# Kernel tuning notes

Measured on AMD Instinct MI355X. Metric: run time of the kernel, lower is better.

Reference implementation:

```python
import jax, jax.numpy as jnp
import numpy as np

N = 100000
E = 1600000
NEG_SLOPE = 0.2


def _gat_layer(x, src, dst, W, a_src, a_dst, b, heads, out_ch):
    n = x.shape[0]
    h = (x @ W).reshape(n, heads, out_ch)                      # [N,H,C]
    alpha_src = (h * a_src).sum(-1)                            # [N,H]
    alpha_dst = (h * a_dst).sum(-1)                            # [N,H]
    e = jax.nn.leaky_relu(alpha_src[src] + alpha_dst[dst], NEG_SLOPE)  # [E,H]
    # segment softmax over incoming edges of each destination node
    m = jax.ops.segment_max(e, dst, num_segments=n)            # [N,H]
    ex = jnp.exp(e - m[dst])
    denom = jax.ops.segment_sum(ex, dst, num_segments=n)       # [N,H]
    alpha = ex / (denom[dst] + 1e-16)                          # [E,H]
    msg = h[src] * alpha[:, :, None]                           # [E,H,C]
    out = jax.ops.segment_sum(msg, dst, num_segments=n)        # [N,H,C]
    return out.reshape(n, heads * out_ch) + b


def setup_inputs() -> dict:
    key = jax.random.key(0)
    ks = jax.random.split(key, 10)
    glorot = lambda k, shape: jax.random.normal(k, shape, jnp.float32) * np.sqrt(2.0 / (shape[0] + shape[-1]))
    x = jax.random.normal(ks[0], (N, 5), jnp.float32)
    edge_index = jax.random.randint(ks[1], (2, E), 0, N, jnp.int64)
    return {
        "x": x,
        "edge_index": edge_index,
        "W1": glorot(ks[2], (5, 64)),
        "a_src1": glorot(ks[3], (8, 8)),
        "a_dst1": glorot(ks[4], (8, 8)),
        "b1": jnp.zeros((64,), jnp.float32),
        "W2": glorot(ks[5], (64, 2)),
        "a_src2": glorot(ks[6], (1, 2)),
        "a_dst2": glorot(ks[7], (1, 2)),
        "b2": jnp.zeros((2,), jnp.float32),
    }


def reference(x, edge_index, W1, a_src1, a_dst1, b1, W2, a_src2, a_dst2, b2):
    n = x.shape[0]
    loop = jnp.arange(n, dtype=edge_index.dtype)
    src = jnp.concatenate([edge_index[0], loop])   # PyG GATConv adds self-loops
    dst = jnp.concatenate([edge_index[1], loop])
    # dropout layers are no-ops in eval mode
    h = jax.nn.elu(_gat_layer(x, src, dst, W1, a_src1, a_dst1, b1, heads=8, out_ch=8))
    out = _gat_layer(h, src, dst, W2, a_src2, a_dst2, b2, heads=1, out_ch=2)
    return jax.nn.log_softmax(out, axis=1)
```

## Files before the change

kernel.cpp:

```cpp
#include <hip/hip_runtime.h>
#include <hip/hip_fp16.h>
#include <math.h>
#include <stdint.h>

#define N_NODES 100000
#define N_EDGES 1600000
#define N_TOT   (N_EDGES + N_NODES)
#define NEG_SLOPE 0.2f
#define LOG2E 1.44269504088896340736f

#define CB     128
#define CBBITS 7
#define NCB    ((N_NODES + CB - 1) / CB)
#define TP     2048
#define NPB    ((N_EDGES + TP - 1) / TP)
#define WINB   2560

typedef int nt_int4 __attribute__((ext_vector_type(4)));

__global__ void k_node1(const float* __restrict__ x, const float* __restrict__ W1,
                        const float* __restrict__ a_src1, const float* __restrict__ a_dst1,
                        __half* __restrict__ xh, __half* __restrict__ as1h,
                        float* __restrict__ ad1) {
    int tid  = blockIdx.x * blockDim.x + threadIdx.x;
    int n    = tid >> 3;
    int head = tid & 7;
    if (n >= N_NODES) return;

    float xv[5];
#pragma unroll
    for (int k = 0; k < 5; ++k) xv[k] = x[n * 5 + k];

    float as = 0.f, ad = 0.f;
#pragma unroll
    for (int j = 0; j < 8; ++j) {
        int c = head * 8 + j;
        float acc = 0.f;
#pragma unroll
        for (int k = 0; k < 5; ++k) acc += xv[k] * W1[k * 64 + c];
        as += acc * a_src1[c];
        ad += acc * a_dst1[c];
    }
    as1h[n * 8 + head] = __float2half(as * LOG2E);
    ad1[n * 8 + head] = ad * LOG2E;

    if (head == 0) {
        __half2 p0 = __halves2half2(__float2half(xv[0]), __float2half(xv[1]));
        __half2 p1 = __halves2half2(__float2half(xv[2]), __float2half(xv[3]));
        __half2 p2 = __halves2half2(__float2half(xv[4]), __float2half(0.f));
        __half2 p3 = __halves2half2(__float2half(0.f), __float2half(0.f));
        __half2* xp = (__half2*)&xh[(size_t)n * 8];
        xp[0] = p0; xp[1] = p1; xp[2] = p2; xp[3] = p3;
    }
}

__global__ void __launch_bounds__(512) k_part(
        const int* __restrict__ src, const int* __restrict__ dst,
        int* __restrict__ ofsT, unsigned* __restrict__ pairs) {
    __shared__ int lcnt[1024];
    __shared__ int sm[512];
    __shared__ unsigned stage[TP];
    int blk = blockIdx.x;
    int t = threadIdx.x;
    int base = blk * TP + t * 4;
    bool act = base < N_EDGES;
    int nE = min(TP, N_EDGES - blk * TP);

    lcnt[t] = 0; lcnt[t + 512] = 0;
    __syncthreads();

    nt_int4 s4, d4;
    if (act) {
        s4 = __builtin_nontemporal_load((const nt_int4*)(src + base));
        d4 = __builtin_nontemporal_load((const nt_int4*)(dst + base));
#pragma unroll
        for (int j = 0; j < 4; ++j) atomicAdd(&lcnt[d4[j] >> CBBITS], 1);
    }
    __syncthreads();

    int b0 = lcnt[t * 2], b1 = lcnt[t * 2 + 1];
    int local = b0 + b1;
    sm[t] = local;
    __syncthreads();
    for (int off = 1; off < 512; off <<= 1) {
        int u = (t >= off) ? sm[t - off] : 0;
        __syncthreads();
        sm[t] += u;
        __syncthreads();
    }
    int run = sm[t] - local;
    lcnt[t * 2] = run; lcnt[t * 2 + 1] = run + b0;
    if (t * 2     <= NCB) ofsT[(size_t)(t * 2)     * NPB + blk] = run;
    if (t * 2 + 1 <= NCB) ofsT[(size_t)(t * 2 + 1) * NPB + blk] = run + b0;
    __syncthreads();

    if (act) {
#pragma unroll
        for (int j = 0; j < 4; ++j) {
            int d = d4[j], s = s4[j];
            int bin = d >> CBBITS;
            int idx = atomicAdd(&lcnt[bin], 1);
            stage[idx] = ((unsigned)(d & (CB - 1)) << 17) | (unsigned)s;
        }
    }
    __syncthreads();
    for (int i = t; i < nE; i += 512)
        pairs[(size_t)blk * TP + i] = stage[i];
}

__global__ void __launch_bounds__(512) k_csr(
        const int* __restrict__ ofsT, const unsigned* __restrict__ pairs,
        int* __restrict__ rbeg, int* __restrict__ rend, int* __restrict__ ssrc) {
    __shared__ unsigned stIn[WINB];
    __shared__ int stOut[WINB];
    __shared__ int lcnt[CB], lofs[CB], lcur[CB];
    __shared__ int wsum[2];
    __shared__ int acur;
    int B = blockIdx.x, t = threadIdx.x;
    int nvalid = min(CB, N_NODES - B * CB);
    int obase = B * WINB;

    if (t < CB) {
        lcnt[t] = (t < nvalid) ? 1 : 0;
        lcur[t] = 1;
    }
    if (t == 0) acur = 0;
    __syncthreads();

    for (int blk = t; blk < NPB; blk += 512) {
        int o0 = ofsT[(size_t)B       * NPB + blk];
        int o1 = ofsT[(size_t)(B + 1) * NPB + blk];
        int n = o1 - o0;
        if (n > 0) {
            int p = atomicAdd(&acur, n);
            const unsigned* pp = pairs + (size_t)blk * TP + o0;
            for (int i = 0; i < n; ++i) {
                unsigned r = pp[i];
                stIn[p + i] = r;
                atomicAdd(&lcnt[r >> 17], 1);
            }
        }
    }
    __syncthreads();
    int m = acur;

    int v = (t < CB) ? lcnt[t] : 0;
    int ln = t & 63, wv = t >> 6;
    int sc = v;
#pragma unroll
    for (int off = 1; off < 64; off <<= 1) {
        int u = __shfl_up(sc, off, 64);
        if (ln >= off) sc += u;
    }
    if (ln == 63 && wv < 2) wsum[wv] = sc;
    __syncthreads();
    int wbase = (wv == 1) ? wsum[0] : 0;
    int ex = wbase + sc - v;
    if (t < CB) {
        lofs[t] = ex;
        int gi = B * CB + t;
        if (gi < N_NODES) {
            rbeg[gi] = obase + ex;
            rend[gi] = obase + ex + v;
            stOut[ex] = gi;
        }
    }
    __syncthreads();

    for (int k = t; k < m; k += 512) {
        unsigned p = stIn[k];
        int dl = p >> 17;
        int idx = atomicAdd(&lcur[dl], 1);
        stOut[lofs[dl] + idx] = (int)(p & 0x1FFFF);
    }
    __syncthreads();

    int tot = m + nvalid;
    for (int i = t; i < tot; i += 512) ssrc[obase + i] = stOut[i];
}

__global__ void __launch_bounds__(256) k_gather1(
        const int* __restrict__ rbeg, const int* __restrict__ rend,
        const int* __restrict__ ssrc, const float4* __restrict__ xh4,
        const __half* __restrict__ as1h, const float* __restrict__ ad1,
        const float* __restrict__ b1, const float* __restrict__ W1,
        const float* __restrict__ W2,
        const float* __restrict__ a_src2, const float* __restrict__ a_dst2,
        float4* __restrict__ rec) {
    int gtid = blockIdx.x * blockDim.x + threadIdx.x;
    int d      = gtid >> 5;
    int lane32 = threadIdx.x & 31;
    if (d >= N_NODES) return;
    int e = lane32 >> 3;
    int h = lane32 & 7;

    int beg = rbeg[d], end = rend[d];
    float adv = ad1[d * 8 + h];
    float c0 = 0.f, c1 = 0.f, c2 = 0.f, c3 = 0.f, c4 = 0.f, den = 0.f;

    for (int k = beg; k < end; k += 8) {
        int kA = k + e, kB = k + 4 + e;
        bool vA = kA < end, vB = kB < end;
        int sA = ssrc[vA ? kA : beg];
        int sB = ssrc[vB ? kB : beg];
        float eA = __half2float(as1h[sA * 8 + h]);
        float eB = __half2float(as1h[sB * 8 + h]);
        float4 xA = xh4[sA];
        float4 xB = xh4[sB];
        float tA = eA + adv; tA = fmaxf(tA, NEG_SLOPE * tA);
        float tB = eB + adv; tB = fmaxf(tB, NEG_SLOPE * tB);
        float wA = vA ? __builtin_amdgcn_exp2f(tA) : 0.f;
        float wB = vB ? __builtin_amdgcn_exp2f(tB) : 0.f;
        float2 A01 = __half22float2(*(__half2*)&xA.x);
        float2 A23 = __half22float2(*(__half2*)&xA.y);
        float2 A4_ = __half22float2(*(__half2*)&xA.z);
        float2 B01 = __half22float2(*(__half2*)&xB.x);
        float2 B23 = __half22float2(*(__half2*)&xB.y);
        float2 B4_ = __half22float2(*(__half2*)&xB.z);
        c0 += wA * A01.x + wB * B01.x;
        c1 += wA * A01.y + wB * B01.y;
        c2 += wA * A23.x + wB * B23.x;
        c3 += wA * A23.y + wB * B23.y;
        c4 += wA * A4_.x + wB * B4_.x;
        den += wA + wB;
    }

#define REDH(x) x += __shfl_xor(x, 8, 64); x += __shfl_xor(x, 16, 64);
    REDH(c0) REDH(c1) REDH(c2) REDH(c3) REDH(c4) REDH(den)
#undef REDH

    float inv = 1.f / den;
    float xs[5];
    xs[0] = c0 * inv; xs[1] = c1 * inv; xs[2] = c2 * inv;
    xs[3] = c3 * inv; xs[4] = c4 * inv;

    float4 hA = ((const float4*)b1)[2 * h];
    float4 hB = ((const float4*)b1)[2 * h + 1];
#pragma unroll
    for (int c = 0; c < 5; ++c) {
        float xc = xs[c];
        float4 wA = *(const float4*)(W1 + c * 64 + 8 * h);
        float4 wB = *(const float4*)(W1 + c * 64 + 8 * h + 4);
        hA.x += xc * wA.x; hA.y += xc * wA.y; hA.z += xc * wA.z; hA.w += xc * wA.w;
        hB.x += xc * wB.x; hB.y += xc * wB.y; hB.z += xc * wB.z; hB.w += xc * wB.w;
    }
    float v0 = hA.x, v1 = hA.y, v2 = hA.z, v3 = hA.w;
    float v4 = hB.x, v5 = hB.y, v6 = hB.z, v7 = hB.w;
    v0 = (v0 > 0.f) ? v0 : (__expf(v0) - 1.f);
    v1 = (v1 > 0.f) ? v1 : (__expf(v1) - 1.f);
    v2 = (v2 > 0.f) ? v2 : (__expf(v2) - 1.f);
    v3 = (v3 > 0.f) ? v3 : (__expf(v3) - 1.f);
    v4 = (v4 > 0.f) ? v4 : (__expf(v4) - 1.f);
    v5 = (v5 > 0.f) ? v5 : (__expf(v5) - 1.f);
    v6 = (v6 > 0.f) ? v6 : (__expf(v6) - 1.f);
    v7 = (v7 > 0.f) ? v7 : (__expf(v7) - 1.f);

    const float4* w4 = (const float4*)(W2 + h * 16);
    float4 wq0 = w4[0], wq1 = w4[1], wq2 = w4[2], wq3 = w4[3];
    float h20 = v0 * wq0.x + v1 * wq0.z + v2 * wq1.x + v3 * wq1.z
              + v4 * wq2.x + v5 * wq2.z + v6 * wq3.x + v7 * wq3.z;
    float h21 = v0 * wq0.y + v1 * wq0.w + v2 * wq1.y + v3 * wq1.w
              + v4 * wq2.y + v5 * wq2.w + v6 * wq3.y + v7 * wq3.w;
    h20 += __shfl_xor(h20, 1, 64); h20 += __shfl_xor(h20, 2, 64); h20 += __shfl_xor(h20, 4, 64);
    h21 += __shfl_xor(h21, 1, 64); h21 += __shfl_xor(h21, 2, 64); h21 += __shfl_xor(h21, 4, 64);

    if (lane32 == 0) {
        float as2v = h20 * a_src2[0] + h21 * a_src2[1];
        float ad2v = h20 * a_dst2[0] + h21 * a_dst2[1];
        rec[d] = make_float4(h20, h21, as2v, ad2v);
    }
}

__global__ void k_gather2(const int* __restrict__ rbeg, const int* __restrict__ rend,
                          const int* __restrict__ ssrc, const float4* __restrict__ rec,
                          const float* __restrict__ b2, float* __restrict__ out) {
    int gtid = blockIdx.x * blockDim.x + threadIdx.x;
    int d    = gtid >> 4;
    int lane = gtid & 15;
    if (d >= N_NODES) return;

    int beg = rbeg[d], end = rend[d];
    float adv = rec[d].w;
    float n0 = 0.f, n1 = 0.f, den = 0.f;
    int k = beg + lane;
    for (; k + 16 < end; k += 32) {
        int s0 = ssrc[k], s1 = ssrc[k + 16];
        float4 r0 = rec[s0];
        float4 r1 = rec[s1];
        float t0 = r0.z + adv; t0 = fmaxf(t0, NEG_SLOPE * t0);
        float t1 = r1.z + adv; t1 = fmaxf(t1, NEG_SLOPE * t1);
        float w0 = __expf(t0), w1 = __expf(t1);
        n0 += w0 * r0.x + w1 * r1.x;
        n1 += w0 * r0.y + w1 * r1.y;
        den += w0 + w1;
    }
    if (k < end) {
        int s = ssrc[k];
        float4 r = rec[s];
        float t = r.z + adv; t = fmaxf(t, NEG_SLOPE * t);
        float w = __expf(t);
        n0 += w * r.x; n1 += w * r.y; den += w;
    }
#pragma unroll
    for (int off = 8; off; off >>= 1) {
        n0  += __shfl_xor(n0,  off, 16);
        n1  += __shfl_xor(n1,  off, 16);
        den += __shfl_xor(den, off, 16);
    }
    if (lane == 0) {
        float o0 = n0 / den + b2[0];
        float o1 = n1 / den + b2[1];
        float m  = fmaxf(o0, o1);
        float lse = m + __logf(__expf(o0 - m) + __expf(o1 - m));
        out[d * 2 + 0] = o0 - lse;
        out[d * 2 + 1] = o1 - lse;
    }
}

extern "C" void kernel_launch(void* const* d_in, const int* in_sizes, int n_in,
                              void* d_out, int out_size, void* d_ws, size_t ws_size,
                              hipStream_t stream) {
    const float* x      = (const float*)d_in[0];
    const int*   ei     = (const int*)d_in[1];
    const float* W1     = (const float*)d_in[2];
    const float* a_src1 = (const float*)d_in[3];
    const float* a_dst1 = (const float*)d_in[4];
    const float* b1     = (const float*)d_in[5];
    const float* W2     = (const float*)d_in[6];
    const float* a_src2 = (const float*)d_in[7];
    const float* a_dst2 = (const float*)d_in[8];
    const float* b2     = (const float*)d_in[9];
    float* out = (float*)d_out;

    const int* src = ei;
    const int* dst = ei + N_EDGES;

    int* ofsT   = (int*)d_ws;
    int* rbeg   = ofsT + (size_t)(NCB + 1) * NPB;
    int* rend   = rbeg + N_NODES;
    unsigned* pairs = (unsigned*)(rend + N_NODES);
    int* ssrc   = (int*)(pairs + N_EDGES);
    uintptr_t pp = ((uintptr_t)(ssrc + (size_t)NCB * WINB) + 255) & ~(uintptr_t)255;
    float4*   rec  = (float4*)pp;
    float*    ad1  = (float*)(rec + N_NODES);
    __half*   as1h = (__half*)(ad1 + (size_t)N_NODES * 8);
    __half*   xh   = as1h + (size_t)N_NODES * 8;

    k_node1<<<(N_NODES * 8 + 255) / 256, 256, 0, stream>>>(x, W1, a_src1, a_dst1,
                                                           xh, as1h, ad1);
    k_part<<<NPB, 512, 0, stream>>>(src, dst, ofsT, pairs);
    k_csr<<<NCB, 512, 0, stream>>>(ofsT, pairs, rbeg, rend, ssrc);
    k_gather1<<<(N_NODES * 32 + 255) / 256, 256, 0, stream>>>(rbeg, rend, ssrc,
                                                              (const float4*)xh,
                                                              as1h, ad1, b1, W1, W2,
                                                              a_src2, a_dst2, rec);
    k_gather2<<<(N_NODES * 16 + 255) / 256, 256, 0, stream>>>(rbeg, rend, ssrc,
                                                              rec, b2, out);
}
```

Before: 174.3 us.

## Merge node projection into partition kernel and split gather1 epilogue into separate kernel

The per-node layer-1 projection is folded into the edge partition kernel as extra blocks, removing one launch and letting the two independent jobs run concurrently. The dense per-node epilogue (W1 expansion, ELU, W2 projection, layer-2 attention logits) moves out of the edge-gather kernel into a new k_rec kernel. The gather kernel now only writes the normalized 5-wide aggregates to a scratch buffer that aliases the partition workspace. This shortens the gather kernel's tail and register footprint, but adds a launch plus an extra write and read of N*8*6 floats.

```diff
diff --git a/kernel.cpp b/kernel.cpp
--- a/kernel.cpp
+++ b/kernel.cpp
@@ -15,53 +15,57 @@
 #define TP     2048
 #define NPB    ((N_EDGES + TP - 1) / TP)
 #define WINB   2560
+#define NB_NODE1 ((N_NODES * 8 + 511) / 512)
 
 typedef int nt_int4 __attribute__((ext_vector_type(4)));
 
-__global__ void k_node1(const float* __restrict__ x, const float* __restrict__ W1,
-                        const float* __restrict__ a_src1, const float* __restrict__ a_dst1,
-                        __half* __restrict__ xh, __half* __restrict__ as1h,
-                        float* __restrict__ ad1) {
-    int tid  = blockIdx.x * blockDim.x + threadIdx.x;
-    int n    = tid >> 3;
-    int head = tid & 7;
-    if (n >= N_NODES) return;
-
-    float xv[5];
-#pragma unroll
-    for (int k = 0; k < 5; ++k) xv[k] = x[n * 5 + k];
-
-    float as = 0.f, ad = 0.f;
-#pragma unroll
-    for (int j = 0; j < 8; ++j) {
-        int c = head * 8 + j;
-        float acc = 0.f;
-#pragma unroll
-        for (int k = 0; k < 5; ++k) acc += xv[k] * W1[k * 64 + c];
-        as += acc * a_src1[c];
-        ad += acc * a_dst1[c];
-    }
-    as1h[n * 8 + head] = __float2half(as * LOG2E);
-    ad1[n * 8 + head] = ad * LOG2E;
-
-    if (head == 0) {
-        __half2 p0 = __halves2half2(__float2half(xv[0]), __float2half(xv[1]));
-        __half2 p1 = __halves2half2(__float2half(xv[2]), __float2half(xv[3]));
-        __half2 p2 = __halves2half2(__float2half(xv[4]), __float2half(0.f));
-        __half2 p3 = __halves2half2(__float2half(0.f), __float2half(0.f));
-        __half2* xp = (__half2*)&xh[(size_t)n * 8];
-        xp[0] = p0; xp[1] = p1; xp[2] = p2; xp[3] = p3;
-    }
-}
-
-__global__ void __launch_bounds__(512) k_part(
+__global__ void __launch_bounds__(512) k_np(
         const int* __restrict__ src, const int* __restrict__ dst,
-        int* __restrict__ ofsT, unsigned* __restrict__ pairs) {
+        int* __restrict__ ofsT, unsigned* __restrict__ pairs,
+        const float* __restrict__ x, const float* __restrict__ W1,
+        const float* __restrict__ a_src1, const float* __restrict__ a_dst1,
+        __half* __restrict__ xh, __half* __restrict__ as1h,
+        float* __restrict__ ad1) {
     __shared__ int lcnt[1024];
     __shared__ int sm[512];
     __shared__ unsigned stage[TP];
+    int t = threadIdx.x;
+
+    if (blockIdx.x >= NPB) {
+        int gid  = (blockIdx.x - NPB) * 512 + t;
+        int n    = gid >> 3;
+        int head = gid & 7;
+        if (n >= N_NODES) return;
+
+        float xv[5];
+#pragma unroll
+        for (int k = 0; k < 5; ++k) xv[k] = x[n * 5 + k];
+
+        float as = 0.f, ad = 0.f;
+#pragma unroll
+        for (int j = 0; j < 8; ++j) {
+            int c = head * 8 + j;
+            float acc = 0.f;
+#pragma unroll
+            for (int k = 0; k < 5; ++k) acc += xv[k] * W1[k * 64 + c];
+            as += acc * a_src1[c];
+            ad += acc * a_dst1[c];
+        }
+        as1h[n * 8 + head] = __float2half(as * LOG2E);
+        ad1[n * 8 + head] = ad * LOG2E;
+
+        if (head == 0) {
+            __half2 p0 = __halves2half2(__float2half(xv[0]), __float2half(xv[1]));
+            __half2 p1 = __halves2half2(__float2half(xv[2]), __float2half(xv[3]));
+            __half2 p2 = __halves2half2(__float2half(xv[4]), __float2half(0.f));
+            __half2 p3 = __halves2half2(__float2half(0.f), __float2half(0.f));
+            __half2* xp = (__half2*)&xh[(size_t)n * 8];
+            xp[0] = p0; xp[1] = p1; xp[2] = p2; xp[3] = p3;
+        }
+        return;
+    }
+
     int blk = blockIdx.x;
-    int t = threadIdx.x;
     int base = blk * TP + t * 4;
     bool act = base < N_EDGES;
     int nE = min(TP, N_EDGES - blk * TP);
@@ -183,10 +187,7 @@
         const int* __restrict__ rbeg, const int* __restrict__ rend,
         const int* __restrict__ ssrc, const float4* __restrict__ xh4,
         const __half* __restrict__ as1h, const float* __restrict__ ad1,
-        const float* __restrict__ b1, const float* __restrict__ W1,
-        const float* __restrict__ W2,
-        const float* __restrict__ a_src2, const float* __restrict__ a_dst2,
-        float4* __restrict__ rec) {
+        float* __restrict__ xsbuf) {
     int gtid = blockIdx.x * blockDim.x + threadIdx.x;
     int d      = gtid >> 5;
     int lane32 = threadIdx.x & 31;
@@ -229,10 +230,30 @@
     REDH(c0) REDH(c1) REDH(c2) REDH(c3) REDH(c4) REDH(den)
 #undef REDH
 
-    float inv = 1.f / den;
-    float xs[5];
-    xs[0] = c0 * inv; xs[1] = c1 * inv; xs[2] = c2 * inv;
-    xs[3] = c3 * inv; xs[4] = c4 * inv;
+    if (e == 0) {
+        float inv = 1.f / den;
+        float* xp = xsbuf + ((size_t)d * 8 + h) * 6;
+        *(float2*)(xp + 0) = make_float2(c0 * inv, c1 * inv);
+        *(float2*)(xp + 2) = make_float2(c2 * inv, c3 * inv);
+        *(float2*)(xp + 4) = make_float2(c4 * inv, 0.f);
+    }
+}
+
+__global__ void __launch_bounds__(256) k_rec(
+        const float* __restrict__ xsbuf, const float* __restrict__ b1,
+        const float* __restrict__ W1, const float* __restrict__ W2,
+        const float* __restrict__ a_src2, const float* __restrict__ a_dst2,
+        float4* __restrict__ rec) {
+    int gtid = blockIdx.x * blockDim.x + threadIdx.x;
+    int d = gtid >> 3;
+    int h = gtid & 7;
+    if (d >= N_NODES) return;
+
+    const float* xp = xsbuf + ((size_t)d * 8 + h) * 6;
+    float2 p0 = *(const float2*)(xp + 0);
+    float2 p1 = *(const float2*)(xp + 2);
+    float2 p2 = *(const float2*)(xp + 4);
+    float xs[5] = { p0.x, p0.y, p1.x, p1.y, p2.x };
 
     float4 hA = ((const float4*)b1)[2 * h];
     float4 hB = ((const float4*)b1)[2 * h + 1];
@@ -264,7 +285,7 @@
     h20 += __shfl_xor(h20, 1, 64); h20 += __shfl_xor(h20, 2, 64); h20 += __shfl_xor(h20, 4, 64);
     h21 += __shfl_xor(h21, 1, 64); h21 += __shfl_xor(h21, 2, 64); h21 += __shfl_xor(h21, 4, 64);
 
-    if (lane32 == 0) {
+    if (h == 0) {
         float as2v = h20 * a_src2[0] + h21 * a_src2[1];
         float ad2v = h20 * a_dst2[0] + h21 * a_dst2[1];
         rec[d] = make_float4(h20, h21, as2v, ad2v);
@@ -335,25 +356,28 @@
     const int* src = ei;
     const int* dst = ei + N_EDGES;
 
-    int* ofsT   = (int*)d_ws;
-    int* rbeg   = ofsT + (size_t)(NCB + 1) * NPB;
+    int* rbeg   = (int*)d_ws;
     int* rend   = rbeg + N_NODES;
-    unsigned* pairs = (unsigned*)(rend + N_NODES);
-    int* ssrc   = (int*)(pairs + N_EDGES);
+    int* ssrc   = rend + N_NODES;
     uintptr_t pp = ((uintptr_t)(ssrc + (size_t)NCB * WINB) + 255) & ~(uintptr_t)255;
     float4*   rec  = (float4*)pp;
     float*    ad1  = (float*)(rec + N_NODES);
     __half*   as1h = (__half*)(ad1 + (size_t)N_NODES * 8);
     __half*   xh   = as1h + (size_t)N_NODES * 8;
-
-    k_node1<<<(N_NODES * 8 + 255) / 256, 256, 0, stream>>>(x, W1, a_src1, a_dst1,
-                                                           xh, as1h, ad1);
-    k_part<<<NPB, 512, 0, stream>>>(src, dst, ofsT, pairs);
+    uintptr_t rg = ((uintptr_t)(xh + (size_t)N_NODES * 8) + 255) & ~(uintptr_t)255;
+    int*      ofsT  = (int*)rg;
+    unsigned* pairs = (unsigned*)(ofsT + (size_t)(NCB + 1) * NPB);
+    float*    xsbuf = (float*)rg;
+
+    k_np<<<NPB + NB_NODE1, 512, 0, stream>>>(src, dst, ofsT, pairs,
+                                             x, W1, a_src1, a_dst1,
+                                             xh, as1h, ad1);
     k_csr<<<NCB, 512, 0, stream>>>(ofsT, pairs, rbeg, rend, ssrc);
     k_gather1<<<(N_NODES * 32 + 255) / 256, 256, 0, stream>>>(rbeg, rend, ssrc,
                                                               (const float4*)xh,
-                                                              as1h, ad1, b1, W1, W2,
-                                                              a_src2, a_dst2, rec);
+                                                              as1h, ad1, xsbuf);
+    k_rec<<<(N_NODES * 8 + 255) / 256, 256, 0, stream>>>(xsbuf, b1, W1, W2,
+                                                         a_src2, a_dst2, rec);
     k_gather2<<<(N_NODES * 16 + 255) / 256, 256, 0, stream>>>(rbeg, rend, ssrc,
                                                               rec, b2, out);
 }
```

Result: faster. 162.1 us (-7.0%).
